# Kernel optimization log

Measured on AMD Instinct MI355X. Metric: run time of the kernel, lower is better.

## Reference

```python
import jax, jax.numpy as jnp
import numpy as np

B, N_P, N_S = 64, 50, 200
N_NODES = N_P * N_S          # 10000 nodes per graph (jobs x ops)
N_CAND = N_S + 1             # 201 candidates
INPUT_DIM, HIDDEN = 3, 64
NODE_DIM = 2 * HIDDEN        # h_nodes feature dim (=> actor in = 6*HIDDEN)
POOL_DIM = 4 * HIDDEN        # h_pooled dim (mean || max pooling)
H_ACTOR, H_CRITIC = 256, 256


def setup_inputs() -> dict:
    key = jax.random.key(0)
    ks = jax.random.split(key, 16)
    p = lambda k, sh: jax.random.normal(k, sh, jnp.float32) * 0.02
    x = jax.random.normal(ks[0], (B, N_NODES, INPUT_DIM), jnp.float32)
    candidate = jax.random.randint(ks[1], (B, N_CAND), 0, N_NODES)
    mask = jax.random.randint(ks[2], (B, N_CAND), 0, 2) > 0
    mask = mask.at[:, 0].set(True)  # guarantee at least one valid action per row
    return {
        "x": x, "candidate": candidate, "mask": mask,
        "fe_w1": p(ks[3], (INPUT_DIM, HIDDEN)), "fe_b1": jnp.zeros((HIDDEN,), jnp.float32),
        "fe_w2": p(ks[4], (HIDDEN, NODE_DIM)), "fe_b2": jnp.zeros((NODE_DIM,), jnp.float32),
        "a_w1": p(ks[5], (NODE_DIM + POOL_DIM, H_ACTOR)), "a_b1": jnp.zeros((H_ACTOR,), jnp.float32),
        "a_w2": p(ks[6], (H_ACTOR, H_ACTOR)), "a_b2": jnp.zeros((H_ACTOR,), jnp.float32),
        "a_w3": p(ks[7], (H_ACTOR, 1)), "a_b3": jnp.zeros((1,), jnp.float32),
        "c_w1": p(ks[8], (POOL_DIM, H_CRITIC)), "c_b1": jnp.zeros((H_CRITIC,), jnp.float32),
        "c_w2": p(ks[9], (H_CRITIC, H_CRITIC)), "c_b2": jnp.zeros((H_CRITIC,), jnp.float32),
        "c_w3": p(ks[10], (H_CRITIC, 1)), "c_b3": jnp.zeros((1,), jnp.float32),
    }


def _actor_critic(x, candidate, mask,
                  fe_w1, fe_b1, fe_w2, fe_b2,
                  a_w1, a_b1, a_w2, a_b2, a_w3, a_b3,
                  c_w1, c_b1, c_w2, c_b2, c_w3, c_b3):
    # --- feature_extract: per-node MLP embedding, graph-level pooling ---
    h = jax.nn.relu(jnp.einsum('bni,ih->bnh', x, fe_w1) + fe_b1)
    h_nodes = jax.nn.relu(jnp.einsum('bnh,hd->bnd', h, fe_w2) + fe_b2)   # [B, N, 2H]
    h_pooled = jnp.concatenate([h_nodes.mean(axis=1), h_nodes.max(axis=1)], axis=-1)  # [B, 4H]

    # --- gather candidate node features (torch.gather over node axis) ---
    cand_feat = jnp.take_along_axis(h_nodes, candidate[:, :, None], axis=1)  # [B, C, 2H]

    # --- concat broadcast pooled feature ---
    pooled_rep = jnp.broadcast_to(h_pooled[:, None, :], (cand_feat.shape[0], cand_feat.shape[1], h_pooled.shape[-1]))
    concat_fea = jnp.concatenate([cand_feat, pooled_rep], axis=-1)  # [B, C, 6H]

    # --- actor MLP (tanh hidden layers, linear out) ---
    a = jnp.tanh(concat_fea @ a_w1 + a_b1)
    a = jnp.tanh(a @ a_w2 + a_b2)
    scores = a @ a_w3 + a_b3                                    # [B, C, 1]

    # --- mask with -inf, softmax over candidate axis ---
    scores = jnp.where(mask[:, :, None], scores, -jnp.inf)
    pi = jax.nn.softmax(scores, axis=1)                          # [B, C, 1]

    # --- critic MLP on pooled feature ---
    c = jnp.tanh(h_pooled @ c_w1 + c_b1)
    c = jnp.tanh(c @ c_w2 + c_b2)
    v = c @ c_w3 + c_b3                                          # [B, 1]
    return pi, v


def reference(x, candidate, mask,
              fe_w1, fe_b1, fe_w2, fe_b2,
              a_w1, a_b1, a_w2, a_b2, a_w3, a_b3,
              c_w1, c_b1, c_w2, c_b2, c_w3, c_b3):
    return _actor_critic(x, candidate, mask,
                         fe_w1, fe_b1, fe_w2, fe_b2,
                         a_w1, a_b1, a_w2, a_b2, a_w3, a_b3,
                         c_w1, c_b1, c_w2, c_b2, c_w3, c_b3)
```

## Files before the change

kernel.cpp:

```cpp
#include <hip/hip_runtime.h>

#define NN 10000
#define NCAND 201
#define NB 64

typedef __attribute__((ext_vector_type(8))) short short8;
typedef __attribute__((ext_vector_type(4))) float f32x4;

__device__ __forceinline__ float bf2f(unsigned short u) {
  return __uint_as_float(((unsigned int)u) << 16);
}
__device__ __forceinline__ unsigned short f2bf(float f) {
  unsigned int u = __float_as_uint(f);
  u += 0x7FFFu + ((u >> 16) & 1u);
  return (unsigned short)(u >> 16);
}
__device__ __forceinline__ float fast_tanh(float x) {
  return 1.0f - 2.0f / (__expf(2.0f * x) + 1.0f);
}
__device__ __forceinline__ float gld(const void* p, long i, int f) {
  return f ? ((const float*)p)[i] : bf2f(((const unsigned short*)p)[i]);
}

__global__ __launch_bounds__(256, 4)
void mega_kernel(const void* __restrict__ x, const int* __restrict__ cand,
                 const void* w1, const void* b1, const void* w2, const void* b2,
                 const void* aw1, const void* ab1, const void* aw2, const void* ab2,
                 const void* aw3, const void* ab3,
                 const void* cw1, const void* cb1, const void* cw2, const void* cb2,
                 const void* cw3, const void* cb3,
                 const unsigned int* mask_w, const unsigned int* cand_w,
                 int* F, int* scnt,
                 float* __restrict__ psumP, float* __restrict__ pmaxP,
                 unsigned short* __restrict__ cfw,
                 unsigned short* __restrict__ aw1t, unsigned short* __restrict__ aw2t,
                 unsigned short* __restrict__ cw1t, unsigned short* __restrict__ cw2t) {
  __shared__ __align__(16) unsigned short pool[128 * 72];
  __shared__ float w1f[3 * 64];
  __shared__ float b1f[64];
  __shared__ float b2f[128];
  __shared__ int cnts[8];

  const int t = threadIdx.x;
  const int j = blockIdx.x;
  const int lane = t & 63;
  const int wv = t >> 6;

  if (j < 1472) {
    if (t < 8) cnts[t] = 0;
    __syncthreads();
    {
      if ((((const unsigned short*)x)[t] & 0x7F80u) >= 0x4300u) atomicAdd(&cnts[0], 1);
      if (t < 192 && (((const unsigned short*)w1)[t] & 0x7F80u) >= 0x4300u) atomicAdd(&cnts[1], 1);
      if (t < 64 && (((const unsigned short*)b1)[t] & 0x7F80u) >= 0x4300u) atomicAdd(&cnts[2], 1);
      if (t < 128 && (((const unsigned short*)b2)[t] & 0x7F80u) >= 0x4300u) atomicAdd(&cnts[3], 1);
      if ((((const unsigned short*)w2)[t] & 0x7F80u) >= 0x4300u) atomicAdd(&cnts[4], 1);
      int co = 0;
#pragma unroll
      for (int q = 0; q < 4; ++q) {
        int i = t * 4 + q;
        if ((i & 1) && cand_w[i] != 0u) co = 1;
      }
      if (co) atomicAdd(&cnts[5], 1);
    }
    __syncthreads();
    const int F0 = cnts[0] > 32, F1 = cnts[1] > 24, F2 = cnts[2] > 8;
    const int F4 = cnts[3] > 16, Fw2 = cnts[4] > 32, C64 = cnts[5] == 0;

    if (j < 1024) {
      unsigned short* h1s = pool;
      const int b = j >> 4;
      const int s = j & 15;

      if (t < 192) w1f[t] = gld(w1, t, F1);
      if (t < 64) b1f[t] = gld(b1, t, F2);
      if (t < 128) b2f[t] = gld(b2, t, F4);

      short8 bfr[2][2];
#pragma unroll
      for (int nl = 0; nl < 2; ++nl)
#pragma unroll
        for (int ks = 0; ks < 2; ++ks) {
          int col = wv * 32 + nl * 16 + (lane & 15);
          short8 v;
#pragma unroll
          for (int jj = 0; jj < 8; ++jj) {
            int k = (lane >> 4) * 8 + ks * 32 + jj;
            v[jj] = (short)f2bf(gld(w2, (long)k * 128 + col, Fw2));
          }
          bfr[nl][ks] = v;
        }
      __syncthreads();

      float csum[2] = {0.f, 0.f};
      float cmax[2] = {0.f, 0.f};
      const int m = t & 127;
      const int kg = t >> 7;

      float x0 = 0.f, x1 = 0.f, x2 = 0.f;
      if (s < 79) {
        int nb = s * 128;
        if (m < min(128, NN - nb)) {
          long xo = ((long)b * NN + nb + m) * 3;
          x0 = gld(x, xo, F0); x1 = gld(x, xo + 1, F0); x2 = gld(x, xo + 2, F0);
        }
      }

      for (int c = s; c < 79; c += 16) {
        int nb = c * 128;
        int cnt = (nb + 128 <= NN) ? 128 : (NN - nb);
        const bool full = (cnt == 128);
        if (full) {
#pragma unroll
          for (int blk = 0; blk < 4; ++blk) {
            short8 v;
#pragma unroll
            for (int i = 0; i < 8; ++i) {
              int k = kg * 32 + blk * 8 + i;
              float vv = x0 * w1f[k] + x1 * w1f[64 + k] + x2 * w1f[128 + k] + b1f[k];
              v[i] = (short)f2bf(fmaxf(vv, 0.f));
            }
            *(short8*)(h1s + m * 72 + kg * 32 + blk * 8) = v;
          }
        } else if (m < cnt) {
#pragma unroll
          for (int blk = 0; blk < 4; ++blk) {
            short8 v;
#pragma unroll
            for (int i = 0; i < 8; ++i) {
              int k = kg * 32 + blk * 8 + i;
              float vv = x0 * w1f[k] + x1 * w1f[64 + k] + x2 * w1f[128 + k] + b1f[k];
              v[i] = (short)f2bf(fmaxf(vv, 0.f));
            }
            *(short8*)(h1s + m * 72 + kg * 32 + blk * 8) = v;
          }
        }
        {
          int cn = c + 16;
          float nx0 = 0.f, nx1 = 0.f, nx2 = 0.f;
          if (cn < 79) {
            int nbn = cn * 128;
            if (m < min(128, NN - nbn)) {
              long xo = ((long)b * NN + nbn + m) * 3;
              nx0 = gld(x, xo, F0); nx1 = gld(x, xo + 1, F0); nx2 = gld(x, xo + 2, F0);
            }
          }
          __syncthreads();
          x0 = nx0; x1 = nx1; x2 = nx2;
        }
        if (full) {
#pragma unroll
          for (int mt = 0; mt < 8; ++mt) {
            const unsigned short* ap = h1s + (mt * 16 + (lane & 15)) * 72 + ((lane >> 4) * 8);
            short8 af0 = *(const short8*)(ap);
            short8 af1 = *(const short8*)(ap + 32);
#pragma unroll
            for (int nl = 0; nl < 2; ++nl) {
              f32x4 acc = {0.f, 0.f, 0.f, 0.f};
              acc = __builtin_amdgcn_mfma_f32_16x16x32_bf16(af0, bfr[nl][0], acc, 0, 0, 0);
              acc = __builtin_amdgcn_mfma_f32_16x16x32_bf16(af1, bfr[nl][1], acc, 0, 0, 0);
              int col = wv * 32 + nl * 16 + (lane & 15);
              float bb = b2f[col];
#pragma unroll
              for (int r = 0; r < 4; ++r) {
                float v = fmaxf(acc[r] + bb, 0.f);
                csum[nl] += v;
                cmax[nl] = fmaxf(cmax[nl], v);
              }
            }
          }
        } else {
#pragma unroll
          for (int mt = 0; mt < 8; ++mt) {
            const unsigned short* ap = h1s + (mt * 16 + (lane & 15)) * 72 + ((lane >> 4) * 8);
            short8 af0 = *(const short8*)(ap);
            short8 af1 = *(const short8*)(ap + 32);
#pragma unroll
            for (int nl = 0; nl < 2; ++nl) {
              f32x4 acc = {0.f, 0.f, 0.f, 0.f};
              acc = __builtin_amdgcn_mfma_f32_16x16x32_bf16(af0, bfr[nl][0], acc, 0, 0, 0);
              acc = __builtin_amdgcn_mfma_f32_16x16x32_bf16(af1, bfr[nl][1], acc, 0, 0, 0);
              int col = wv * 32 + nl * 16 + (lane & 15);
              float bb = b2f[col];
#pragma unroll
              for (int r = 0; r < 4; ++r) {
                int row = mt * 16 + ((lane >> 4) * 4) + r;
                if (row < cnt) {
                  float v = fmaxf(acc[r] + bb, 0.f);
                  csum[nl] += v;
                  cmax[nl] = fmaxf(cmax[nl], v);
                }
              }
            }
          }
        }
        __syncthreads();
      }
#pragma unroll
      for (int nl = 0; nl < 2; ++nl) {
        csum[nl] += __shfl_xor(csum[nl], 16);
        csum[nl] += __shfl_xor(csum[nl], 32);
        cmax[nl] = fmaxf(cmax[nl], __shfl_xor(cmax[nl], 16));
        cmax[nl] = fmaxf(cmax[nl], __shfl_xor(cmax[nl], 32));
      }
      if (lane < 16) {
#pragma unroll
        for (int nl = 0; nl < 2; ++nl) {
          int col = wv * 32 + nl * 16 + lane;
          psumP[((long)b * 16 + s) * 128 + col] = csum[nl];
          pmaxP[((long)b * 16 + s) * 128 + col] = cmax[nl];
        }
      }
    } else {
      unsigned short* h1c = pool;
      const int idx = j - 1024;
      const int b = idx / 7;
      const int cb = idx % 7;
      const int cbase = cb * 29;

      if (t < 128) b2f[t] = gld(b2, t, F4);

      {
        int r = t & 31;
        int ci = cbase + r;
        if (ci > NCAND - 1) ci = NCAND - 1;
        long cidx = (long)b * NCAND + ci;
        int nd = C64 ? cand[2 * cidx] : cand[cidx];
        long xo = ((long)b * NN + nd) * 3;
        float x0 = gld(x, xo, F0), x1 = gld(x, xo + 1, F0), x2 = gld(x, xo + 2, F0);
        int kg = t >> 5;
#pragma unroll
        for (int i = 0; i < 8; ++i) {
          int k = kg * 8 + i;
          float v = x0 * gld(w1, k, F1) + x1 * gld(w1, 64 + k, F1) +
                    x2 * gld(w1, 128 + k, F1) + gld(b1, k, F2);
          h1c[r * 72 + k] = f2bf(fmaxf(v, 0.f));
        }
      }
      __syncthreads();

      {
        short8 af[2][2];
#pragma unroll
        for (int mt = 0; mt < 2; ++mt)
#pragma unroll
          for (int ks = 0; ks < 2; ++ks)
            af[mt][ks] = *(const short8*)(h1c + (mt * 16 + (lane & 15)) * 72 + ((lane >> 4) * 8) + ks * 32);
#pragma unroll
        for (int nl = 0; nl < 2; ++nl) {
          int col = wv * 32 + nl * 16 + (lane & 15);
          short8 bf0, bf1;
#pragma unroll
          for (int jj = 0; jj < 8; ++jj) {
            int k = (lane >> 4) * 8 + jj;
            bf0[jj] = (short)f2bf(gld(w2, (long)k * 128 + col, Fw2));
            bf1[jj] = (short)f2bf(gld(w2, (long)(k + 32) * 128 + col, Fw2));
          }
          float bb = b2f[col];
#pragma unroll
          for (int mt = 0; mt < 2; ++mt) {
            f32x4 acc = {0.f, 0.f, 0.f, 0.f};
            acc = __builtin_amdgcn_mfma_f32_16x16x32_bf16(af[mt][0], bf0, acc, 0, 0, 0);
            acc = __builtin_amdgcn_mfma_f32_16x16x32_bf16(af[mt][1], bf1, acc, 0, 0, 0);
#pragma unroll
            for (int r = 0; r < 4; ++r) {
              int row = mt * 16 + ((lane >> 4) * 4) + r;
              cfw[(long)idx * 4096 + row * 128 + col] = f2bf(fmaxf(acc[r] + bb, 0.f));
            }
          }
        }
      }
    }
    return;
  }

  if (t < 8) cnts[t] = 0;
  __syncthreads();

  if (j < 1856) {
    const unsigned short* pa = (const unsigned short*)aw1;
    const unsigned short* pb = (const unsigned short*)aw2;
    const unsigned short* pc = (const unsigned short*)cw1;
    const unsigned short* pd = (const unsigned short*)cw2;
    if ((pa[t] & 0x7F80u) >= 0x4300u) atomicAdd(&cnts[0], 1);
    if ((pb[t] & 0x7F80u) >= 0x4300u) atomicAdd(&cnts[1], 1);
    if ((pc[t] & 0x7F80u) >= 0x4300u) atomicAdd(&cnts[2], 1);
    if ((pd[t] & 0x7F80u) >= 0x4300u) atomicAdd(&cnts[3], 1);
    __syncthreads();
    const int Faw1 = cnts[0] > 32, Faw2 = cnts[1] > 32;
    const int Fcw1 = cnts[2] > 32, Fcw2 = cnts[3] > 32;
    int i = (j - 1472) * 256 + t;
    if (i < 256 * 384) { int n = i / 384, k = i % 384; aw1t[i] = f2bf(gld(aw1, k * 256 + n, Faw1)); }
    if (i < 256 * 256) {
      int n = i >> 8, k = i & 255;
      aw2t[i] = f2bf(gld(aw2, k * 256 + n, Faw2));
      cw1t[i] = f2bf(gld(cw1, k * 256 + n, Fcw1));
      cw2t[i] = f2bf(gld(cw2, k * 256 + n, Fcw2));
    }
  } else if (j < 1873) {
    const void* ptrs[17] = {x, w1, b1, w2, b2, aw1, ab1, aw2, ab2, aw3, ab3,
                            cw1, cb1, cw2, cb2, cw3, cb3};
    const int sizes[17] = {1920000, 192, 64, 8192, 128, 98304, 256, 65536, 256,
                           256, 1, 65536, 256, 65536, 256, 256, 1};
    int a = j - 1856;
    const unsigned short* p = (const unsigned short*)ptrs[a];
    int K = min(sizes[a], 2048);
    int c = 0;
    for (int i = t; i < K; i += 256)
      if ((p[i] & 0x7F80u) >= 0x4300u) c++;
    if (c) atomicAdd(&cnts[0], c);
    __syncthreads();
    if (t == 0) F[a] = (cnts[0] > (K >> 3)) ? 1 : 0;
  } else if (j == 1873) {
    int flo = 0, fhi = 0, fgt = 0;
    for (int i = t; i < 3216; i += 256) {
      unsigned int w = mask_w[i];
      if ((w & 0xFFFFu) == 0x3F80u) flo = 1;
      if ((w >> 16) == 0x3F80u) fhi = 1;
      if (w > 1u) fgt = 1;
    }
    if (flo) cnts[0] = 1;
    if (fhi) cnts[1] = 1;
    if (fgt) cnts[2] = 1;
    __syncthreads();
    if (t == 0) F[17] = cnts[0] ? 2 : (cnts[1] ? 3 : (cnts[2] ? 1 : 0));
  } else {
    int co = 0;
    for (int i = t; i < 1024; i += 256)
      if ((i & 1) && cand_w[i] != 0u) co = 1;
    if (co) cnts[0] = 1;
    if (t < 64) scnt[t] = 0;
    __syncthreads();
    if (t == 0) F[18] = cnts[0] ? 0 : 1;
  }
}

__global__ __launch_bounds__(256)
void actorB_kernel(const unsigned short* __restrict__ cfw,
                   const void* __restrict__ ab1, const void* __restrict__ ab2,
                   const void* __restrict__ aw3, const void* __restrict__ ab3,
                   const void* __restrict__ mask,
                   const int* __restrict__ F,
                   const float* __restrict__ psumP, const float* __restrict__ pmaxP,
                   const unsigned short* __restrict__ aw1t,
                   const unsigned short* __restrict__ aw2t,
                   const unsigned short* __restrict__ cw1t,
                   const unsigned short* __restrict__ cw2t,
                   const void* __restrict__ cb1, const void* __restrict__ cb2,
                   const void* __restrict__ cw3, const void* __restrict__ cb3,
                   float* __restrict__ scores, int* __restrict__ scnt,
                   void* __restrict__ out) {
  __shared__ __align__(16) unsigned short a1s[32 * 264];
  __shared__ __align__(16) unsigned short a2s[32 * 264];
  __shared__ float pactS[256], ab2f[256], plfS[256];
  __shared__ float red[4];
  __shared__ int amLast;

  const int t = threadIdx.x;
  const int lane = t & 63;
  const int wv = t >> 6;

  if (blockIdx.x >= 448) {
    const int b = blockIdx.x - 448;
    float ssum = 0.f, smax = 0.f;
    if (t < 128) {
#pragma unroll
      for (int sl = 0; sl < 16; ++sl) {
        ssum += psumP[((long)b * 16 + sl) * 128 + t];
        smax = fmaxf(smax, pmaxP[((long)b * 16 + sl) * 128 + t]);
      }
      plfS[t] = ssum * (1.0f / 10000.0f);
      plfS[128 + t] = smax;
    }
    const int OF = (F[0] + F[1] + F[3] + F[5] + F[7] + F[9] + F[11] + F[13] + F[15]) >= 5;
    const int F12 = F[12], F14 = F[14], F15 = F[15], F16 = F[16];
    __syncthreads();
    {
      float a = gld(cb1, t, F12);
      const unsigned short* row = cw1t + t * 256;
#pragma unroll
      for (int k8 = 0; k8 < 32; ++k8) {
        short8 w = *(const short8*)(row + k8 * 8);
#pragma unroll
        for (int j = 0; j < 8; ++j)
          a += plfS[k8 * 8 + j] * bf2f((unsigned short)w[j]);
      }
      ab2f[t] = fast_tanh(a);
    }
    __syncthreads();
    {
      float a2 = gld(cb2, t, F14);
      const unsigned short* row = cw2t + t * 256;
#pragma unroll
      for (int k8 = 0; k8 < 32; ++k8) {
        short8 w = *(const short8*)(row + k8 * 8);
#pragma unroll
        for (int j = 0; j < 8; ++j)
          a2 += ab2f[k8 * 8 + j] * bf2f((unsigned short)w[j]);
      }
      a2 = fast_tanh(a2);
      float p = a2 * gld(cw3, t, F15);
      for (int o = 32; o; o >>= 1) p += __shfl_xor(p, o);
      __syncthreads();
      if (lane == 0) red[wv] = p;
      __syncthreads();
      if (t == 0) {
        float v = red[0] + red[1] + red[2] + red[3] + gld(cb3, 0, F16);
        if (!(v == v)) v = 0.f;
        if (OF) ((float*)out)[NB * NCAND + b] = v;
        else ((unsigned short*)out)[NB * NCAND + b] = f2bf(v);
      }
    }
    return;
  }

  const int b = blockIdx.x / 7;
  const int cb = blockIdx.x % 7;
  const int cbase = cb * 29;
  const int cntc = min(29, NCAND - cbase);
  const int F6 = F[6], F8 = F[8], F9 = F[9], F10 = F[10];

  {
    float ssum = 0.f, smax = 0.f;
    if (t < 128) {
#pragma unroll
      for (int sl = 0; sl < 16; ++sl) {
        ssum += psumP[((long)b * 16 + sl) * 128 + t];
        smax = fmaxf(smax, pmaxP[((long)b * 16 + sl) * 128 + t]);
      }
      plfS[t] = bf2f(f2bf(ssum * (1.0f / 10000.0f)));
      plfS[128 + t] = bf2f(f2bf(smax));
    }
  }
  ab2f[t] = gld(ab2, t, F8);
  __syncthreads();

  float pa = gld(ab1, t, F6);
  {
    const unsigned short* row = aw1t + t * 384 + 128;
#pragma unroll
    for (int k8 = 0; k8 < 32; ++k8) {
      short8 w = *(const short8*)(row + k8 * 8);
#pragma unroll
      for (int j = 0; j < 8; ++j)
        pa += plfS[k8 * 8 + j] * bf2f((unsigned short)w[j]);
    }
  }

  {
    f32x4 acc[2][4];
#pragma unroll
    for (int mt = 0; mt < 2; ++mt)
#pragma unroll
      for (int nt = 0; nt < 4; ++nt) acc[mt][nt] = (f32x4){0.f, 0.f, 0.f, 0.f};
    const unsigned short* cfb = cfw + (long)blockIdx.x * 4096;
#pragma unroll
    for (int ks = 0; ks < 4; ++ks) {
      short8 af0 = *(const short8*)(cfb + (lane & 15) * 128 + ks * 32 + ((lane >> 4) * 8));
      short8 af1 = *(const short8*)(cfb + (16 + (lane & 15)) * 128 + ks * 32 + ((lane >> 4) * 8));
#pragma unroll
      for (int nt = 0; nt < 4; ++nt) {
        int col = wv * 64 + nt * 16 + (lane & 15);
        short8 bfr = *(const short8*)(aw1t + col * 384 + ks * 32 + ((lane >> 4) * 8));
        acc[0][nt] = __builtin_amdgcn_mfma_f32_16x16x32_bf16(af0, bfr, acc[0][nt], 0, 0, 0);
        acc[1][nt] = __builtin_amdgcn_mfma_f32_16x16x32_bf16(af1, bfr, acc[1][nt], 0, 0, 0);
      }
    }
    pactS[t] = pa;
    __syncthreads();
#pragma unroll
    for (int mt = 0; mt < 2; ++mt)
#pragma unroll
      for (int nt = 0; nt < 4; ++nt) {
        int col = wv * 64 + nt * 16 + (lane & 15);
        float bb = pactS[col];
#pragma unroll
        for (int r = 0; r < 4; ++r) {
          int row = mt * 16 + ((lane >> 4) * 4) + r;
          a1s[row * 264 + col] = f2bf(fast_tanh(acc[mt][nt][r] + bb));
        }
      }
  }
  __syncthreads();

  {
    f32x4 acc[2][4];
#pragma unroll
    for (int mt = 0; mt < 2; ++mt)
#pragma unroll
      for (int nt = 0; nt < 4; ++nt) acc[mt][nt] = (f32x4){0.f, 0.f, 0.f, 0.f};
    for (int ks = 0; ks < 8; ++ks) {
      short8 af0 = *(const short8*)(a1s + (lane & 15) * 264 + ks * 32 + ((lane >> 4) * 8));
      short8 af1 = *(const short8*)(a1s + (16 + (lane & 15)) * 264 + ks * 32 + ((lane >> 4) * 8));
#pragma unroll
      for (int nt = 0; nt < 4; ++nt) {
        int col = wv * 64 + nt * 16 + (lane & 15);
        short8 bfr = *(const short8*)(aw2t + col * 256 + ks * 32 + ((lane >> 4) * 8));
        acc[0][nt] = __builtin_amdgcn_mfma_f32_16x16x32_bf16(af0, bfr, acc[0][nt], 0, 0, 0);
        acc[1][nt] = __builtin_amdgcn_mfma_f32_16x16x32_bf16(af1, bfr, acc[1][nt], 0, 0, 0);
      }
    }
#pragma unroll
    for (int mt = 0; mt < 2; ++mt)
#pragma unroll
      for (int nt = 0; nt < 4; ++nt) {
        int col = wv * 64 + nt * 16 + (lane & 15);
        float bb = ab2f[col];
#pragma unroll
        for (int r = 0; r < 4; ++r) {
          int row = mt * 16 + ((lane >> 4) * 4) + r;
          a2s[row * 264 + col] = f2bf(fast_tanh(acc[mt][nt][r] + bb));
        }
      }
  }
  __syncthreads();

  {
    int row = t >> 3, seg = t & 7;
    float p = 0.f;
#pragma unroll 8
    for (int i = 0; i < 32; ++i) {
      int k = seg * 32 + i;
      p += bf2f(a2s[row * 264 + k]) * gld(aw3, k, F9);
    }
    p += __shfl_xor(p, 1);
    p += __shfl_xor(p, 2);
    p += __shfl_xor(p, 4);
    if (seg == 0 && row < cntc)
      atomicExch(&scores[b * 256 + cbase + row], p + gld(ab3, 0, F10));
  }
  __syncthreads();

  if (t == 0) {
    __threadfence();
    amLast = (atomicAdd(&scnt[b], 1) == 6);
  }
  __syncthreads();
  if (!amLast) return;

  const int MM = F[17];
  const int OF = (F[0] + F[1] + F[3] + F[5] + F[7] + F[9] + F[11] + F[13] + F[15]) >= 5;
  float sraw = 0.f, sv = -1e30f;
  bool valid = false;
  if (t < NCAND) {
    sraw = atomicAdd(&scores[b * 256 + t], 0.0f);
    long idx = (long)b * NCAND + t;
    if (MM == 0)      valid = ((const int*)mask)[idx] != 0;
    else if (MM == 1) valid = ((const unsigned char*)mask)[idx] != 0;
    else if (MM == 2) valid = ((const unsigned short*)mask)[idx] != 0;
    else              valid = ((const unsigned int*)mask)[idx] != 0;
    if (valid) sv = sraw;
  }
  float m = sv;
  for (int o = 32; o; o >>= 1) m = fmaxf(m, __shfl_xor(m, o));
  if (lane == 0) red[wv] = m;
  __syncthreads();
  m = fmaxf(fmaxf(red[0], red[1]), fmaxf(red[2], red[3]));
  __syncthreads();
  float e = valid ? __expf(sraw - m) : 0.f;
  if (!(e == e)) e = 0.f;
  float ss = e;
  for (int o = 32; o; o >>= 1) ss += __shfl_xor(ss, o);
  if (lane == 0) red[wv] = ss;
  __syncthreads();
  float tot = red[0] + red[1] + red[2] + red[3];
  tot = fmaxf(tot, 1e-30f);
  if (t < NCAND) {
    float pv = e / tot;
    if (!(pv == pv)) pv = 0.f;
    if (OF) ((float*)out)[b * NCAND + t] = pv;
    else ((unsigned short*)out)[b * NCAND + t] = f2bf(pv);
  }
}

extern "C" void kernel_launch(void* const* d_in, const int* in_sizes, int n_in,
                              void* d_out, int out_size, void* d_ws, size_t ws_size,
                              hipStream_t stream) {
  const void* x = d_in[0];
  const int* cand = (const int*)d_in[1];
  const void* mask = d_in[2];
  const void* fe_w1 = d_in[3];
  const void* fe_b1 = d_in[4];
  const void* fe_w2 = d_in[5];
  const void* fe_b2 = d_in[6];
  const void* a_w1 = d_in[7];
  const void* a_b1 = d_in[8];
  const void* a_w2 = d_in[9];
  const void* a_b2 = d_in[10];
  const void* a_w3 = d_in[11];
  const void* a_b3 = d_in[12];
  const void* c_w1 = d_in[13];
  const void* c_b1 = d_in[14];
  const void* c_w2 = d_in[15];
  const void* c_b2 = d_in[16];
  const void* c_w3 = d_in[17];
  const void* c_b3 = d_in[18];

  char* ws = (char*)d_ws;
  float* scores = (float*)(ws + 65536);
  unsigned short* aw1t = (unsigned short*)(ws + 147456);
  unsigned short* aw2t = (unsigned short*)(ws + 344064);
  int* F = (int*)(ws + 475136);
  unsigned short* cw1t = (unsigned short*)(ws + 475264);
  unsigned short* cw2t = (unsigned short*)(ws + 606336);
  unsigned short* cfw = (unsigned short*)(ws + 802944);
  int* scnt = (int*)(ws + 4472960);
  float* psumP = (float*)(ws + 4473216);
  float* pmaxP = (float*)(ws + 4997504);

  mega_kernel<<<1875, 256, 0, stream>>>(x, cand, fe_w1, fe_b1, fe_w2, fe_b2,
                                        a_w1, a_b1, a_w2, a_b2, a_w3, a_b3,
                                        c_w1, c_b1, c_w2, c_b2, c_w3, c_b3,
                                        (const unsigned int*)mask,
                                        (const unsigned int*)cand, F, scnt,
                                        psumP, pmaxP, cfw, aw1t, aw2t, cw1t, cw2t);
  actorB_kernel<<<512, 256, 0, stream>>>(cfw, a_b1, a_b2, a_w3, a_b3, mask, F,
                                         psumP, pmaxP, aw1t, aw2t, cw1t, cw2t,
                                         c_b1, c_b2, c_w3, c_b3,
                                         scores, scnt, (void*)d_out);
}
```

Measured before the change: 162.1 us.

## Drop critic weight transposes and read original weights with coalesced column access

The critic weight matrices are no longer transposed into workspace bf16 copies in the first kernel. The critic MLP and the pooled part of actor layer 1 now read the original row-major weights directly, with each thread taking one output column so that loads coalesce across threads. The pooled-feature reduction is split across all 256 threads (sum for half, max for the other half), and the second kernel gets a launch-bounds occupancy hint. This removes transpose work and workspace traffic from the first kernel, but now every actor block re-reads a 256x256 slice of the original, possibly fp32, weights using scalar loads.

```diff
diff --git a/kernel.cpp b/kernel.cpp
--- a/kernel.cpp
+++ b/kernel.cpp
@@ -33,8 +33,7 @@
                  int* F, int* scnt,
                  float* __restrict__ psumP, float* __restrict__ pmaxP,
                  unsigned short* __restrict__ cfw,
-                 unsigned short* __restrict__ aw1t, unsigned short* __restrict__ aw2t,
-                 unsigned short* __restrict__ cw1t, unsigned short* __restrict__ cw2t) {
+                 unsigned short* __restrict__ aw1t, unsigned short* __restrict__ aw2t) {
   __shared__ __align__(16) unsigned short pool[128 * 72];
   __shared__ float w1f[3 * 64];
   __shared__ float b1f[64];
@@ -280,22 +279,15 @@
   if (j < 1856) {
     const unsigned short* pa = (const unsigned short*)aw1;
     const unsigned short* pb = (const unsigned short*)aw2;
-    const unsigned short* pc = (const unsigned short*)cw1;
-    const unsigned short* pd = (const unsigned short*)cw2;
     if ((pa[t] & 0x7F80u) >= 0x4300u) atomicAdd(&cnts[0], 1);
     if ((pb[t] & 0x7F80u) >= 0x4300u) atomicAdd(&cnts[1], 1);
-    if ((pc[t] & 0x7F80u) >= 0x4300u) atomicAdd(&cnts[2], 1);
-    if ((pd[t] & 0x7F80u) >= 0x4300u) atomicAdd(&cnts[3], 1);
     __syncthreads();
     const int Faw1 = cnts[0] > 32, Faw2 = cnts[1] > 32;
-    const int Fcw1 = cnts[2] > 32, Fcw2 = cnts[3] > 32;
     int i = (j - 1472) * 256 + t;
     if (i < 256 * 384) { int n = i / 384, k = i % 384; aw1t[i] = f2bf(gld(aw1, k * 256 + n, Faw1)); }
     if (i < 256 * 256) {
       int n = i >> 8, k = i & 255;
       aw2t[i] = f2bf(gld(aw2, k * 256 + n, Faw2));
-      cw1t[i] = f2bf(gld(cw1, k * 256 + n, Fcw1));
-      cw2t[i] = f2bf(gld(cw2, k * 256 + n, Fcw2));
     }
   } else if (j < 1873) {
     const void* ptrs[17] = {x, w1, b1, w2, b2, aw1, ab1, aw2, ab2, aw3, ab3,
@@ -335,18 +327,18 @@
   }
 }
 
-__global__ __launch_bounds__(256)
+__global__ __launch_bounds__(256, 4)
 void actorB_kernel(const unsigned short* __restrict__ cfw,
-                   const void* __restrict__ ab1, const void* __restrict__ ab2,
+                   const void* __restrict__ aw1, const void* __restrict__ ab1,
+                   const void* __restrict__ ab2,
                    const void* __restrict__ aw3, const void* __restrict__ ab3,
                    const void* __restrict__ mask,
                    const int* __restrict__ F,
                    const float* __restrict__ psumP, const float* __restrict__ pmaxP,
                    const unsigned short* __restrict__ aw1t,
                    const unsigned short* __restrict__ aw2t,
-                   const unsigned short* __restrict__ cw1t,
-                   const unsigned short* __restrict__ cw2t,
-                   const void* __restrict__ cb1, const void* __restrict__ cb2,
+                   const void* __restrict__ cw1, const void* __restrict__ cb1,
+                   const void* __restrict__ cw2, const void* __restrict__ cb2,
                    const void* __restrict__ cw3, const void* __restrict__ cb3,
                    float* __restrict__ scores, int* __restrict__ scnt,
                    void* __restrict__ out) {
@@ -360,44 +352,42 @@
   const int lane = t & 63;
   const int wv = t >> 6;
 
+  float pr = 0.f;
+  {
+    const int b = (blockIdx.x < 448) ? (blockIdx.x / 7) : (blockIdx.x - 448);
+    const int col = t & 127;
+    if (t < 128) {
+#pragma unroll
+      for (int sl = 0; sl < 16; ++sl)
+        pr += psumP[((long)b * 16 + sl) * 128 + col];
+      pr *= (1.0f / 10000.0f);
+    } else {
+#pragma unroll
+      for (int sl = 0; sl < 16; ++sl)
+        pr = fmaxf(pr, pmaxP[((long)b * 16 + sl) * 128 + col]);
+    }
+  }
+
   if (blockIdx.x >= 448) {
     const int b = blockIdx.x - 448;
-    float ssum = 0.f, smax = 0.f;
-    if (t < 128) {
-#pragma unroll
-      for (int sl = 0; sl < 16; ++sl) {
-        ssum += psumP[((long)b * 16 + sl) * 128 + t];
-        smax = fmaxf(smax, pmaxP[((long)b * 16 + sl) * 128 + t]);
-      }
-      plfS[t] = ssum * (1.0f / 10000.0f);
-      plfS[128 + t] = smax;
-    }
+    plfS[t] = pr;
     const int OF = (F[0] + F[1] + F[3] + F[5] + F[7] + F[9] + F[11] + F[13] + F[15]) >= 5;
-    const int F12 = F[12], F14 = F[14], F15 = F[15], F16 = F[16];
+    const int F11 = F[11], F12 = F[12], F13 = F[13];
+    const int F14 = F[14], F15 = F[15], F16 = F[16];
     __syncthreads();
     {
       float a = gld(cb1, t, F12);
-      const unsigned short* row = cw1t + t * 256;
-#pragma unroll
-      for (int k8 = 0; k8 < 32; ++k8) {
-        short8 w = *(const short8*)(row + k8 * 8);
-#pragma unroll
-        for (int j = 0; j < 8; ++j)
-          a += plfS[k8 * 8 + j] * bf2f((unsigned short)w[j]);
-      }
+#pragma unroll 8
+      for (int k = 0; k < 256; ++k)
+        a += plfS[k] * gld(cw1, (long)k * 256 + t, F11);
       ab2f[t] = fast_tanh(a);
     }
     __syncthreads();
     {
       float a2 = gld(cb2, t, F14);
-      const unsigned short* row = cw2t + t * 256;
-#pragma unroll
-      for (int k8 = 0; k8 < 32; ++k8) {
-        short8 w = *(const short8*)(row + k8 * 8);
-#pragma unroll
-        for (int j = 0; j < 8; ++j)
-          a2 += ab2f[k8 * 8 + j] * bf2f((unsigned short)w[j]);
-      }
+#pragma unroll 8
+      for (int k = 0; k < 256; ++k)
+        a2 += ab2f[k] * gld(cw2, (long)k * 256 + t, F13);
       a2 = fast_tanh(a2);
       float p = a2 * gld(cw3, t, F15);
       for (int o = 32; o; o >>= 1) p += __shfl_xor(p, o);
@@ -418,34 +408,16 @@
   const int cb = blockIdx.x % 7;
   const int cbase = cb * 29;
   const int cntc = min(29, NCAND - cbase);
-  const int F6 = F[6], F8 = F[8], F9 = F[9], F10 = F[10];
-
-  {
-    float ssum = 0.f, smax = 0.f;
-    if (t < 128) {
-#pragma unroll
-      for (int sl = 0; sl < 16; ++sl) {
-        ssum += psumP[((long)b * 16 + sl) * 128 + t];
-        smax = fmaxf(smax, pmaxP[((long)b * 16 + sl) * 128 + t]);
-      }
-      plfS[t] = bf2f(f2bf(ssum * (1.0f / 10000.0f)));
-      plfS[128 + t] = bf2f(f2bf(smax));
-    }
-  }
+  const int F5 = F[5], F6 = F[6], F8 = F[8], F9 = F[9], F10 = F[10];
+
+  plfS[t] = bf2f(f2bf(pr));
   ab2f[t] = gld(ab2, t, F8);
   __syncthreads();
 
   float pa = gld(ab1, t, F6);
-  {
-    const unsigned short* row = aw1t + t * 384 + 128;
-#pragma unroll
-    for (int k8 = 0; k8 < 32; ++k8) {
-      short8 w = *(const short8*)(row + k8 * 8);
-#pragma unroll
-      for (int j = 0; j < 8; ++j)
-        pa += plfS[k8 * 8 + j] * bf2f((unsigned short)w[j]);
-    }
-  }
+#pragma unroll 8
+  for (int k = 0; k < 256; ++k)
+    pa += plfS[k] * gld(aw1, (long)(128 + k) * 256 + t, F5);
 
   {
     f32x4 acc[2][4];
@@ -601,8 +573,6 @@
   unsigned short* aw1t = (unsigned short*)(ws + 147456);
   unsigned short* aw2t = (unsigned short*)(ws + 344064);
   int* F = (int*)(ws + 475136);
-  unsigned short* cw1t = (unsigned short*)(ws + 475264);
-  unsigned short* cw2t = (unsigned short*)(ws + 606336);
   unsigned short* cfw = (unsigned short*)(ws + 802944);
   int* scnt = (int*)(ws + 4472960);
   float* psumP = (float*)(ws + 4473216);
@@ -613,9 +583,9 @@
                                         c_w1, c_b1, c_w2, c_b2, c_w3, c_b3,
                                         (const unsigned int*)mask,
                                         (const unsigned int*)cand, F, scnt,
-                                        psumP, pmaxP, cfw, aw1t, aw2t, cw1t, cw2t);
-  actorB_kernel<<<512, 256, 0, stream>>>(cfw, a_b1, a_b2, a_w3, a_b3, mask, F,
-                                         psumP, pmaxP, aw1t, aw2t, cw1t, cw2t,
-                                         c_b1, c_b2, c_w3, c_b3,
+                                        psumP, pmaxP, cfw, aw1t, aw2t);
+  actorB_kernel<<<512, 256, 0, stream>>>(cfw, a_w1, a_b1, a_b2, a_w3, a_b3,
+                                         mask, F, psumP, pmaxP, aw1t, aw2t,
+                                         c_w1, c_b1, c_w2, c_b2, c_w3, c_b3,
                                          scores, scnt, (void*)d_out);
 }
```

New measurement: 163.4 us. About the same (+0.8%).

## Fold pooled-feature projection into MFMA accumulation and split pool reduction across threads

Applied to the files above, without the earlier changes.

Replaces the scalar per-thread dot product of the pooled features against the actor's first-layer weights with extra MFMA steps. These add the broadcast pooled row directly into every candidate row's accumulator, and the bias is applied at the epilogue. The pooled sum and max reductions are now split across all 256 threads (sum in one half, max in the other) rather than 128 threads each doing both. The change also sets launch bounds to 4 blocks and partially unrolls the critic loops. This adds MFMA work on the duplicated pooled row and drops one barrier, in exchange for removing a long scalar FMA loop.

```diff
diff --git a/kernel.cpp b/kernel.cpp
--- a/kernel.cpp
+++ b/kernel.cpp
@@ -335,7 +335,7 @@
   }
 }
 
-__global__ __launch_bounds__(256)
+__global__ __launch_bounds__(256, 4)
 void actorB_kernel(const unsigned short* __restrict__ cfw,
                    const void* __restrict__ ab1, const void* __restrict__ ab2,
                    const void* __restrict__ aw3, const void* __restrict__ ab3,
@@ -352,7 +352,8 @@
                    void* __restrict__ out) {
   __shared__ __align__(16) unsigned short a1s[32 * 264];
   __shared__ __align__(16) unsigned short a2s[32 * 264];
-  __shared__ float pactS[256], ab2f[256], plfS[256];
+  __shared__ __align__(16) unsigned short plfB[256];
+  __shared__ float ab1f[256], ab2f[256], plfS[256];
   __shared__ float red[4];
   __shared__ int amLast;
 
@@ -360,25 +361,32 @@
   const int lane = t & 63;
   const int wv = t >> 6;
 
+  float pr = 0.f;
+  {
+    const int b = (blockIdx.x < 448) ? (blockIdx.x / 7) : (blockIdx.x - 448);
+    const int col = t & 127;
+    if (t < 128) {
+#pragma unroll
+      for (int sl = 0; sl < 16; ++sl)
+        pr += psumP[((long)b * 16 + sl) * 128 + col];
+      pr *= (1.0f / 10000.0f);
+    } else {
+#pragma unroll
+      for (int sl = 0; sl < 16; ++sl)
+        pr = fmaxf(pr, pmaxP[((long)b * 16 + sl) * 128 + col]);
+    }
+  }
+
   if (blockIdx.x >= 448) {
     const int b = blockIdx.x - 448;
-    float ssum = 0.f, smax = 0.f;
-    if (t < 128) {
-#pragma unroll
-      for (int sl = 0; sl < 16; ++sl) {
-        ssum += psumP[((long)b * 16 + sl) * 128 + t];
-        smax = fmaxf(smax, pmaxP[((long)b * 16 + sl) * 128 + t]);
-      }
-      plfS[t] = ssum * (1.0f / 10000.0f);
-      plfS[128 + t] = smax;
-    }
+    plfS[t] = pr;
     const int OF = (F[0] + F[1] + F[3] + F[5] + F[7] + F[9] + F[11] + F[13] + F[15]) >= 5;
     const int F12 = F[12], F14 = F[14], F15 = F[15], F16 = F[16];
     __syncthreads();
     {
       float a = gld(cb1, t, F12);
       const unsigned short* row = cw1t + t * 256;
-#pragma unroll
+#pragma unroll 4
       for (int k8 = 0; k8 < 32; ++k8) {
         short8 w = *(const short8*)(row + k8 * 8);
 #pragma unroll
@@ -391,7 +399,7 @@
     {
       float a2 = gld(cb2, t, F14);
       const unsigned short* row = cw2t + t * 256;
-#pragma unroll
+#pragma unroll 4
       for (int k8 = 0; k8 < 32; ++k8) {
         short8 w = *(const short8*)(row + k8 * 8);
 #pragma unroll
@@ -420,32 +428,10 @@
   const int cntc = min(29, NCAND - cbase);
   const int F6 = F[6], F8 = F[8], F9 = F[9], F10 = F[10];
 
-  {
-    float ssum = 0.f, smax = 0.f;
-    if (t < 128) {
-#pragma unroll
-      for (int sl = 0; sl < 16; ++sl) {
-        ssum += psumP[((long)b * 16 + sl) * 128 + t];
-        smax = fmaxf(smax, pmaxP[((long)b * 16 + sl) * 128 + t]);
-      }
-      plfS[t] = bf2f(f2bf(ssum * (1.0f / 10000.0f)));
-      plfS[128 + t] = bf2f(f2bf(smax));
-    }
-  }
+  plfB[t] = f2bf(pr);
+  ab1f[t] = gld(ab1, t, F6);
   ab2f[t] = gld(ab2, t, F8);
   __syncthreads();
-
-  float pa = gld(ab1, t, F6);
-  {
-    const unsigned short* row = aw1t + t * 384 + 128;
-#pragma unroll
-    for (int k8 = 0; k8 < 32; ++k8) {
-      short8 w = *(const short8*)(row + k8 * 8);
-#pragma unroll
-      for (int j = 0; j < 8; ++j)
-        pa += plfS[k8 * 8 + j] * bf2f((unsigned short)w[j]);
-    }
-  }
 
   {
     f32x4 acc[2][4];
@@ -466,14 +452,23 @@
         acc[1][nt] = __builtin_amdgcn_mfma_f32_16x16x32_bf16(af1, bfr, acc[1][nt], 0, 0, 0);
       }
     }
-    pactS[t] = pa;
-    __syncthreads();
-#pragma unroll
-    for (int mt = 0; mt < 2; ++mt)
+#pragma unroll
+    for (int ks = 0; ks < 8; ++ks) {
+      short8 afp = *(const short8*)(plfB + ks * 32 + ((lane >> 4) * 8));
 #pragma unroll
       for (int nt = 0; nt < 4; ++nt) {
         int col = wv * 64 + nt * 16 + (lane & 15);
-        float bb = pactS[col];
+        short8 bfr = *(const short8*)(aw1t + col * 384 + 128 + ks * 32 + ((lane >> 4) * 8));
+        acc[0][nt] = __builtin_amdgcn_mfma_f32_16x16x32_bf16(afp, bfr, acc[0][nt], 0, 0, 0);
+        acc[1][nt] = __builtin_amdgcn_mfma_f32_16x16x32_bf16(afp, bfr, acc[1][nt], 0, 0, 0);
+      }
+    }
+#pragma unroll
+    for (int mt = 0; mt < 2; ++mt)
+#pragma unroll
+      for (int nt = 0; nt < 4; ++nt) {
+        int col = wv * 64 + nt * 16 + (lane & 15);
+        float bb = ab1f[col];
 #pragma unroll
         for (int r = 0; r < 4; ++r) {
           int row = mt * 16 + ((lane >> 4) * 4) + r;
```

After: 156.0 us. 3.8% less time.

## Share pooled actor-bias projection across candidate blocks via flag; fold critic into block

Applied to the files above, without the earlier changes.

The per-batch pooled projection through the actor's first layer was recomputed by all 7 candidate blocks of a batch. Now block cb==0 computes it once and publishes it to global memory with a ready flag, and the other blocks spin-wait on the flag after their first MFMA phase, with a fallback that recomputes it on timeout. The separate 64 critic blocks are folded into the cb==1 blocks, so the grid shrinks from 512 to 448, and the psum/pmax partials are staged through shared memory with vector loads. Inter-block spin waiting risks stalls if producer blocks are not resident, and the critic work now adds latency to one block per batch.

```diff
diff --git a/kernel.cpp b/kernel.cpp
--- a/kernel.cpp
+++ b/kernel.cpp
@@ -30,7 +30,7 @@
                  const void* cw1, const void* cb1, const void* cw2, const void* cb2,
                  const void* cw3, const void* cb3,
                  const unsigned int* mask_w, const unsigned int* cand_w,
-                 int* F, int* scnt,
+                 int* F, int* scnt, int* pflag,
                  float* __restrict__ psumP, float* __restrict__ pmaxP,
                  unsigned short* __restrict__ cfw,
                  unsigned short* __restrict__ aw1t, unsigned short* __restrict__ aw2t,
@@ -330,18 +330,20 @@
       if ((i & 1) && cand_w[i] != 0u) co = 1;
     if (co) cnts[0] = 1;
     if (t < 64) scnt[t] = 0;
+    if (t >= 64 && t < 128) pflag[t - 64] = 0;
     __syncthreads();
     if (t == 0) F[18] = cnts[0] ? 0 : 1;
   }
 }
 
-__global__ __launch_bounds__(256)
+__global__ __launch_bounds__(256, 4)
 void actorB_kernel(const unsigned short* __restrict__ cfw,
                    const void* __restrict__ ab1, const void* __restrict__ ab2,
                    const void* __restrict__ aw3, const void* __restrict__ ab3,
                    const void* __restrict__ mask,
                    const int* __restrict__ F,
                    const float* __restrict__ psumP, const float* __restrict__ pmaxP,
+                   float* __restrict__ pact, int* __restrict__ pflag,
                    const unsigned short* __restrict__ aw1t,
                    const unsigned short* __restrict__ aw2t,
                    const unsigned short* __restrict__ cw1t,
@@ -352,38 +354,103 @@
                    void* __restrict__ out) {
   __shared__ __align__(16) unsigned short a1s[32 * 264];
   __shared__ __align__(16) unsigned short a2s[32 * 264];
-  __shared__ float pactS[256], ab2f[256], plfS[256];
+  __shared__ float pactS[256], ab2f[256];
   __shared__ float red[4];
   __shared__ int amLast;
+  __shared__ int pready;
 
   const int t = threadIdx.x;
+  const int b = blockIdx.x / 7;
+  const int cb = blockIdx.x % 7;
+  const int cbase = cb * 29;
+  const int cntc = min(29, NCAND - cbase);
   const int lane = t & 63;
   const int wv = t >> 6;
-
-  if (blockIdx.x >= 448) {
-    const int b = blockIdx.x - 448;
-    float ssum = 0.f, smax = 0.f;
-    if (t < 128) {
-#pragma unroll
-      for (int sl = 0; sl < 16; ++sl) {
-        ssum += psumP[((long)b * 16 + sl) * 128 + t];
-        smax = fmaxf(smax, pmaxP[((long)b * 16 + sl) * 128 + t]);
-      }
-      plfS[t] = ssum * (1.0f / 10000.0f);
-      plfS[128 + t] = smax;
-    }
+  const int F8 = F[8], F9 = F[9], F10 = F[10];
+
+  float* stgS = (float*)a1s;
+  float* stgM = (float*)a2s;
+
+  if (cb == 0) {
+    const int F6 = F[6];
+    {
+      const float4* ps = (const float4*)(psumP + (long)b * 2048);
+      const float4* pm = (const float4*)(pmaxP + (long)b * 2048);
+      ((float4*)stgS)[t * 2] = ps[t * 2];
+      ((float4*)stgS)[t * 2 + 1] = ps[t * 2 + 1];
+      ((float4*)stgM)[t * 2] = pm[t * 2];
+      ((float4*)stgM)[t * 2 + 1] = pm[t * 2 + 1];
+    }
+    __syncthreads();
+    {
+      float r = 0.f;
+      if (t < 128) {
+#pragma unroll
+        for (int sl = 0; sl < 16; ++sl) r += stgS[sl * 128 + t];
+        r = bf2f(f2bf(r * (1.0f / 10000.0f)));
+      } else {
+        const int c = t - 128;
+#pragma unroll
+        for (int sl = 0; sl < 16; ++sl) r = fmaxf(r, stgM[sl * 128 + c]);
+        r = bf2f(f2bf(r));
+      }
+      pactS[t] = r;
+    }
+    __syncthreads();
+    float a = gld(ab1, t, F6);
+    {
+      const unsigned short* row = aw1t + t * 384 + 128;
+#pragma unroll 4
+      for (int k8 = 0; k8 < 32; ++k8) {
+        short8 w = *(const short8*)(row + k8 * 8);
+#pragma unroll
+        for (int jj = 0; jj < 8; ++jj)
+          a += pactS[k8 * 8 + jj] * bf2f((unsigned short)w[jj]);
+      }
+    }
+    __syncthreads();
+    pactS[t] = a;
+    atomicExch(&pact[(long)b * 256 + t], a);
+    __syncthreads();
+    if (t == 0) {
+      __threadfence();
+      atomicExch(&pflag[b], 1);
+    }
+  } else if (cb == 1) {
     const int OF = (F[0] + F[1] + F[3] + F[5] + F[7] + F[9] + F[11] + F[13] + F[15]) >= 5;
     const int F12 = F[12], F14 = F[14], F15 = F[15], F16 = F[16];
+    {
+      const float4* ps = (const float4*)(psumP + (long)b * 2048);
+      const float4* pm = (const float4*)(pmaxP + (long)b * 2048);
+      ((float4*)stgS)[t * 2] = ps[t * 2];
+      ((float4*)stgS)[t * 2 + 1] = ps[t * 2 + 1];
+      ((float4*)stgM)[t * 2] = pm[t * 2];
+      ((float4*)stgM)[t * 2 + 1] = pm[t * 2 + 1];
+    }
+    __syncthreads();
+    {
+      float r = 0.f;
+      if (t < 128) {
+#pragma unroll
+        for (int sl = 0; sl < 16; ++sl) r += stgS[sl * 128 + t];
+        r *= (1.0f / 10000.0f);
+      } else {
+        const int c = t - 128;
+#pragma unroll
+        for (int sl = 0; sl < 16; ++sl) r = fmaxf(r, stgM[sl * 128 + c]);
+      }
+      pactS[t] = r;
+    }
     __syncthreads();
     {
       float a = gld(cb1, t, F12);
       const unsigned short* row = cw1t + t * 256;
-#pragma unroll
+#pragma unroll 4
       for (int k8 = 0; k8 < 32; ++k8) {
         short8 w = *(const short8*)(row + k8 * 8);
 #pragma unroll
-        for (int j = 0; j < 8; ++j)
-          a += plfS[k8 * 8 + j] * bf2f((unsigned short)w[j]);
+        for (int jj = 0; jj < 8; ++jj)
+          a += pactS[k8 * 8 + jj] * bf2f((unsigned short)w[jj]);
       }
       ab2f[t] = fast_tanh(a);
     }
@@ -391,17 +458,16 @@
     {
       float a2 = gld(cb2, t, F14);
       const unsigned short* row = cw2t + t * 256;
-#pragma unroll
+#pragma unroll 4
       for (int k8 = 0; k8 < 32; ++k8) {
         short8 w = *(const short8*)(row + k8 * 8);
 #pragma unroll
-        for (int j = 0; j < 8; ++j)
-          a2 += ab2f[k8 * 8 + j] * bf2f((unsigned short)w[j]);
+        for (int jj = 0; jj < 8; ++jj)
+          a2 += ab2f[k8 * 8 + jj] * bf2f((unsigned short)w[jj]);
       }
       a2 = fast_tanh(a2);
       float p = a2 * gld(cw3, t, F15);
       for (int o = 32; o; o >>= 1) p += __shfl_xor(p, o);
-      __syncthreads();
       if (lane == 0) red[wv] = p;
       __syncthreads();
       if (t == 0) {
@@ -410,49 +476,16 @@
         if (OF) ((float*)out)[NB * NCAND + b] = v;
         else ((unsigned short*)out)[NB * NCAND + b] = f2bf(v);
       }
-    }
-    return;
-  }
-
-  const int b = blockIdx.x / 7;
-  const int cb = blockIdx.x % 7;
-  const int cbase = cb * 29;
-  const int cntc = min(29, NCAND - cbase);
-  const int F6 = F[6], F8 = F[8], F9 = F[9], F10 = F[10];
-
+      __syncthreads();
+    }
+  }
+
+  f32x4 acc[2][4];
+#pragma unroll
+  for (int mt = 0; mt < 2; ++mt)
+#pragma unroll
+    for (int nt = 0; nt < 4; ++nt) acc[mt][nt] = (f32x4){0.f, 0.f, 0.f, 0.f};
   {
-    float ssum = 0.f, smax = 0.f;
-    if (t < 128) {
-#pragma unroll
-      for (int sl = 0; sl < 16; ++sl) {
-        ssum += psumP[((long)b * 16 + sl) * 128 + t];
-        smax = fmaxf(smax, pmaxP[((long)b * 16 + sl) * 128 + t]);
-      }
-      plfS[t] = bf2f(f2bf(ssum * (1.0f / 10000.0f)));
-      plfS[128 + t] = bf2f(f2bf(smax));
-    }
-  }
-  ab2f[t] = gld(ab2, t, F8);
-  __syncthreads();
-
-  float pa = gld(ab1, t, F6);
-  {
-    const unsigned short* row = aw1t + t * 384 + 128;
-#pragma unroll
-    for (int k8 = 0; k8 < 32; ++k8) {
-      short8 w = *(const short8*)(row + k8 * 8);
-#pragma unroll
-      for (int j = 0; j < 8; ++j)
-        pa += plfS[k8 * 8 + j] * bf2f((unsigned short)w[j]);
-    }
-  }
-
-  {
-    f32x4 acc[2][4];
-#pragma unroll
-    for (int mt = 0; mt < 2; ++mt)
-#pragma unroll
-      for (int nt = 0; nt < 4; ++nt) acc[mt][nt] = (f32x4){0.f, 0.f, 0.f, 0.f};
     const unsigned short* cfb = cfw + (long)blockIdx.x * 4096;
 #pragma unroll
     for (int ks = 0; ks < 4; ++ks) {
@@ -466,29 +499,86 @@
         acc[1][nt] = __builtin_amdgcn_mfma_f32_16x16x32_bf16(af1, bfr, acc[1][nt], 0, 0, 0);
       }
     }
-    pactS[t] = pa;
-    __syncthreads();
+  }
+
+  if (cb != 0) {
+    if (t == 0) {
+      int ok = 1, spins = 0;
+      while (atomicAdd(&pflag[b], 0) == 0) {
+        if (++spins > 100000) { ok = 0; break; }
+        __builtin_amdgcn_s_sleep(2);
+      }
+      pready = ok;
+    }
+    __syncthreads();
+    if (pready) {
+      pactS[t] = atomicAdd(&pact[(long)b * 256 + t], 0.0f);
+    } else {
+      const int F6 = F[6];
+      {
+        const float4* ps = (const float4*)(psumP + (long)b * 2048);
+        const float4* pm = (const float4*)(pmaxP + (long)b * 2048);
+        ((float4*)stgS)[t * 2] = ps[t * 2];
+        ((float4*)stgS)[t * 2 + 1] = ps[t * 2 + 1];
+        ((float4*)stgM)[t * 2] = pm[t * 2];
+        ((float4*)stgM)[t * 2 + 1] = pm[t * 2 + 1];
+      }
+      __syncthreads();
+      {
+        float r = 0.f;
+        if (t < 128) {
+#pragma unroll
+          for (int sl = 0; sl < 16; ++sl) r += stgS[sl * 128 + t];
+          r = bf2f(f2bf(r * (1.0f / 10000.0f)));
+        } else {
+          const int c = t - 128;
+#pragma unroll
+          for (int sl = 0; sl < 16; ++sl) r = fmaxf(r, stgM[sl * 128 + c]);
+          r = bf2f(f2bf(r));
+        }
+        ab2f[t] = r;
+      }
+      __syncthreads();
+      float a = gld(ab1, t, F6);
+      {
+        const unsigned short* row = aw1t + t * 384 + 128;
+#pragma unroll 4
+        for (int k8 = 0; k8 < 32; ++k8) {
+          short8 w = *(const short8*)(row + k8 * 8);
+#pragma unroll
+          for (int jj = 0; jj < 8; ++jj)
+            a += ab2f[k8 * 8 + jj] * bf2f((unsigned short)w[jj]);
+        }
+      }
+      __syncthreads();
+      pactS[t] = a;
+    }
+    __syncthreads();
+  }
+
+  ab2f[t] = gld(ab2, t, F8);
+  __syncthreads();
+
+#pragma unroll
+  for (int mt = 0; mt < 2; ++mt)
+#pragma unroll
+    for (int nt = 0; nt < 4; ++nt) {
+      int col = wv * 64 + nt * 16 + (lane & 15);
+      float bb = pactS[col];
+#pragma unroll
+      for (int r = 0; r < 4; ++r) {
+        int row = mt * 16 + ((lane >> 4) * 4) + r;
+        a1s[row * 264 + col] = f2bf(fast_tanh(acc[mt][nt][r] + bb));
+      }
+    }
+  __syncthreads();
+
+  {
+    f32x4 acc2[2][4];
 #pragma unroll
     for (int mt = 0; mt < 2; ++mt)
 #pragma unroll
-      for (int nt = 0; nt < 4; ++nt) {
-        int col = wv * 64 + nt * 16 + (lane & 15);
-        float bb = pactS[col];
-#pragma unroll
-        for (int r = 0; r < 4; ++r) {
-          int row = mt * 16 + ((lane >> 4) * 4) + r;
-          a1s[row * 264 + col] = f2bf(fast_tanh(acc[mt][nt][r] + bb));
-        }
-      }
-  }
-  __syncthreads();
-
-  {
-    f32x4 acc[2][4];
-#pragma unroll
-    for (int mt = 0; mt < 2; ++mt)
-#pragma unroll
-      for (int nt = 0; nt < 4; ++nt) acc[mt][nt] = (f32x4){0.f, 0.f, 0.f, 0.f};
+      for (int nt = 0; nt < 4; ++nt) acc2[mt][nt] = (f32x4){0.f, 0.f, 0.f, 0.f};
     for (int ks = 0; ks < 8; ++ks) {
       short8 af0 = *(const short8*)(a1s + (lane & 15) * 264 + ks * 32 + ((lane >> 4) * 8));
       short8 af1 = *(const short8*)(a1s + (16 + (lane & 15)) * 264 + ks * 32 + ((lane >> 4) * 8));
@@ -496,8 +586,8 @@
       for (int nt = 0; nt < 4; ++nt) {
         int col = wv * 64 + nt * 16 + (lane & 15);
         short8 bfr = *(const short8*)(aw2t + col * 256 + ks * 32 + ((lane >> 4) * 8));
-        acc[0][nt] = __builtin_amdgcn_mfma_f32_16x16x32_bf16(af0, bfr, acc[0][nt], 0, 0, 0);
-        acc[1][nt] = __builtin_amdgcn_mfma_f32_16x16x32_bf16(af1, bfr, acc[1][nt], 0, 0, 0);
+        acc2[0][nt] = __builtin_amdgcn_mfma_f32_16x16x32_bf16(af0, bfr, acc2[0][nt], 0, 0, 0);
+        acc2[1][nt] = __builtin_amdgcn_mfma_f32_16x16x32_bf16(af1, bfr, acc2[1][nt], 0, 0, 0);
       }
     }
 #pragma unroll
@@ -509,7 +599,7 @@
 #pragma unroll
         for (int r = 0; r < 4; ++r) {
           int row = mt * 16 + ((lane >> 4) * 4) + r;
-          a2s[row * 264 + col] = f2bf(fast_tanh(acc[mt][nt][r] + bb));
+          a2s[row * 264 + col] = f2bf(fast_tanh(acc2[mt][nt][r] + bb));
         }
       }
   }
@@ -597,12 +687,14 @@
   const void* c_b3 = d_in[18];
 
   char* ws = (char*)d_ws;
+  int* pflag = (int*)(ws);
   float* scores = (float*)(ws + 65536);
   unsigned short* aw1t = (unsigned short*)(ws + 147456);
   unsigned short* aw2t = (unsigned short*)(ws + 344064);
   int* F = (int*)(ws + 475136);
   unsigned short* cw1t = (unsigned short*)(ws + 475264);
   unsigned short* cw2t = (unsigned short*)(ws + 606336);
+  float* pact = (float*)(ws + 737408);
   unsigned short* cfw = (unsigned short*)(ws + 802944);
   int* scnt = (int*)(ws + 4472960);
   float* psumP = (float*)(ws + 4473216);
@@ -612,10 +704,11 @@
                                         a_w1, a_b1, a_w2, a_b2, a_w3, a_b3,
                                         c_w1, c_b1, c_w2, c_b2, c_w3, c_b3,
                                         (const unsigned int*)mask,
-                                        (const unsigned int*)cand, F, scnt,
+                                        (const unsigned int*)cand, F, scnt, pflag,
                                         psumP, pmaxP, cfw, aw1t, aw2t, cw1t, cw2t);
-  actorB_kernel<<<512, 256, 0, stream>>>(cfw, a_b1, a_b2, a_w3, a_b3, mask, F,
-                                         psumP, pmaxP, aw1t, aw2t, cw1t, cw2t,
+  actorB_kernel<<<448, 256, 0, stream>>>(cfw, a_b1, a_b2, a_w3, a_b3, mask, F,
+                                         psumP, pmaxP, pact, pflag,
+                                         aw1t, aw2t, cw1t, cw2t,
                                          c_b1, c_b2, c_w3, c_b3,
                                          scores, scnt, (void*)d_out);
 }
```

Measured after the change: 156.7 us (median of 2 runs). 3.4% less time.
